# Kernel tuning notes

Measured on AMD Instinct MI355X. Metric: run time of the kernel, lower is better.

Reference implementation:

```python
import jax, jax.numpy as jnp
import numpy as np

R = 32  # voxel resolution


def setup_inputs() -> dict:
    key = jax.random.key(0)
    k1, k2 = jax.random.split(key)
    B, C, N = 8, 64, 100000
    features = jax.random.normal(k1, (B, C, N), dtype=jnp.float32)
    coords = jax.random.uniform(k2, (B, 3, N), dtype=jnp.float32)  # unit cube [0,1]
    return {"features": features, "coords": coords}


def reference(features, coords):
    # features: [B, C, N], coords: [B, 3, N] in [0, 1]
    B, C, N = features.shape
    norm_coords = jnp.clip(coords * R, 0, R - 1)
    vox_coords = jnp.round(norm_coords).astype(jnp.int32)  # [B, 3, N]

    # flat voxel index per point: x*R^2 + y*R + z, offset per batch
    idx = vox_coords[:, 0] * R * R + vox_coords[:, 1] * R + vox_coords[:, 2]  # [B, N]
    flat_idx = (idx + jnp.arange(B, dtype=jnp.int32)[:, None] * (R ** 3)).reshape(-1)  # [B*N]

    feat = jnp.transpose(features, (0, 2, 1)).reshape(B * N, C)  # [B*N, C]
    sums = jax.ops.segment_sum(feat, flat_idx, num_segments=B * R ** 3)  # [B*R^3, C]
    cnt = jax.ops.segment_sum(jnp.ones((B * N,), features.dtype), flat_idx,
                              num_segments=B * R ** 3)  # [B*R^3]
    avg = sums / jnp.maximum(cnt, 1.0)[:, None]  # average; empty voxels stay 0

    vox_feat = jnp.transpose(avg.reshape(B, R ** 3, C), (0, 2, 1)).reshape(B, C, R, R, R)
    return vox_feat, vox_coords.astype(jnp.int64)
```

## Files before the change

kernel.cpp:

```cpp
#include <hip/hip_runtime.h>

#define RR 32
#define R3 32768
#define BATCH 8
#define CH 64
#define NPTS 100000
#define NPOINTS (BATCH * NPTS)
#define NVOX (BATCH * R3)
#define SCAN_BLOCKS (NVOX / 256)

typedef unsigned int uint32;

__device__ __forceinline__ uint32 f2bf(float f) {
    uint32 u = __float_as_uint(f);
    return (u + 0x7fffu + ((u >> 16) & 1u)) >> 16;
}
__device__ __forceinline__ float bf2f(uint32 h) {
    return __uint_as_float(h << 16);
}

__global__ __launch_bounds__(256) void phase1_count(
    const float* __restrict__ coords,
    uint32* __restrict__ vox,
    uint32* __restrict__ cnt,
    float* __restrict__ out2)
{
    int gid = blockIdx.x * blockDim.x + threadIdx.x;
    if (gid >= NPOINTS) return;
    int b = gid / NPTS;
    int n = gid - b * NPTS;

    const float* cb = coords + (size_t)b * 3 * NPTS + n;
    float fx = fminf(fmaxf(cb[0]        * 32.0f, 0.0f), 31.0f);
    float fy = fminf(fmaxf(cb[NPTS]     * 32.0f, 0.0f), 31.0f);
    float fz = fminf(fmaxf(cb[2 * NPTS] * 32.0f, 0.0f), 31.0f);
    int x = (int)rintf(fx);
    int y = (int)rintf(fy);
    int z = (int)rintf(fz);
    uint32 g = (uint32)(b * R3 + x * (RR * RR) + y * RR + z);

    float* o2 = out2 + (size_t)b * 3 * NPTS + n;
    o2[0]        = (float)x;
    o2[NPTS]     = (float)y;
    o2[2 * NPTS] = (float)z;

    vox[gid] = g;
    atomicAdd(&cnt[g], 1u);
}

__global__ __launch_bounds__(256) void scan_block_sums(
    const uint32* __restrict__ cnt, uint32* __restrict__ bsum)
{
    __shared__ uint32 s[256];
    int t = threadIdx.x;
    s[t] = cnt[blockIdx.x * 256 + t];
    __syncthreads();
    for (int off = 128; off > 0; off >>= 1) {
        if (t < off) s[t] += s[t + off];
        __syncthreads();
    }
    if (t == 0) bsum[blockIdx.x] = s[0];
}

__global__ __launch_bounds__(256) void scan_bsum(uint32* __restrict__ bsum)
{
    __shared__ uint32 s[256];
    int t = threadIdx.x;
    uint32 v0 = bsum[4 * t], v1 = bsum[4 * t + 1], v2 = bsum[4 * t + 2], v3 = bsum[4 * t + 3];
    uint32 tot = v0 + v1 + v2 + v3;
    s[t] = tot;
    __syncthreads();
    for (int off = 1; off < 256; off <<= 1) {
        uint32 x = (t >= off) ? s[t - off] : 0u;
        __syncthreads();
        s[t] += x;
        __syncthreads();
    }
    uint32 excl = s[t] - tot;
    bsum[4 * t]     = excl;
    bsum[4 * t + 1] = excl + v0;
    bsum[4 * t + 2] = excl + v0 + v1;
    bsum[4 * t + 3] = excl + v0 + v1 + v2;
}

__global__ __launch_bounds__(256) void scan_final(
    const uint32* __restrict__ cnt, const uint32* __restrict__ bsum,
    uint32* __restrict__ starts, uint32* __restrict__ cursor)
{
    __shared__ uint32 s[256];
    int t = threadIdx.x;
    int gid = blockIdx.x * 256 + t;
    uint32 v = cnt[gid];
    s[t] = v;
    __syncthreads();
    for (int off = 1; off < 256; off <<= 1) {
        uint32 x = (t >= off) ? s[t - off] : 0u;
        __syncthreads();
        s[t] += x;
        __syncthreads();
    }
    uint32 st = bsum[blockIdx.x] + s[t] - v;
    starts[gid] = st;
    cursor[gid] = st;
}

__global__ __launch_bounds__(256) void phase3_scatter(
    const float* __restrict__ feat,
    const uint32* __restrict__ vox,
    uint32* __restrict__ cursor,
    uint4* __restrict__ sorted)
{
    int gid = blockIdx.x * blockDim.x + threadIdx.x;
    if (gid >= NPOINTS) return;
    int b = gid / NPTS;
    int n = gid - b * NPTS;

    uint32 g = vox[gid];
    uint32 pos = atomicAdd(&cursor[g], 1u);

    const float* frow = feat + (size_t)b * CH * NPTS + n;
    uint4* dst = sorted + (size_t)pos * 8;
#pragma unroll
    for (int j = 0; j < 8; ++j) {
        uint4 w;
        float f0 = frow[(size_t)(8 * j + 0) * NPTS];
        float f1 = frow[(size_t)(8 * j + 1) * NPTS];
        float f2 = frow[(size_t)(8 * j + 2) * NPTS];
        float f3 = frow[(size_t)(8 * j + 3) * NPTS];
        float f4 = frow[(size_t)(8 * j + 4) * NPTS];
        float f5 = frow[(size_t)(8 * j + 5) * NPTS];
        float f6 = frow[(size_t)(8 * j + 6) * NPTS];
        float f7 = frow[(size_t)(8 * j + 7) * NPTS];
        w.x = f2bf(f0) | (f2bf(f1) << 16);
        w.y = f2bf(f2) | (f2bf(f3) << 16);
        w.z = f2bf(f4) | (f2bf(f5) << 16);
        w.w = f2bf(f6) | (f2bf(f7) << 16);
        dst[j] = w;
    }
}

__global__ __launch_bounds__(256) void phase4_reduce(
    const uint32* __restrict__ sorted,
    const uint32* __restrict__ starts,
    float* __restrict__ out1)
{
    __shared__ float tile[64][65];

    int gbase = blockIdx.x * 64;
    int tid = threadIdx.x;
    int wave = tid >> 6, lane = tid & 63;

    if (lane < 32) {
        for (int k = 0; k < 16; ++k) {
            int g = gbase + wave * 16 + k;
            uint32 s = starts[g];
            uint32 e = (g == NVOX - 1) ? (uint32)NPOINTS : starts[g + 1];
            float a0 = 0.0f, a1 = 0.0f;
            for (uint32 p = s; p < e; ++p) {
                uint32 w = sorted[(size_t)p * 32 + lane];
                a0 += bf2f(w & 0xffffu);
                a1 += bf2f(w >> 16);
            }
            uint32 c = e - s;
            float rcp = 1.0f / (float)(c > 1u ? c : 1u);
            int vloc = wave * 16 + k;
            tile[vloc][2 * lane]     = a0 * rcp;
            tile[vloc][2 * lane + 1] = a1 * rcp;
        }
    }
    __syncthreads();

    int b = gbase / R3;
    int v0 = gbase - b * R3;
    int vv = tid & 63;
    int c0 = tid >> 6;
    float* obase = out1 + (size_t)b * CH * R3 + v0 + vv;
#pragma unroll
    for (int jj = 0; jj < 16; ++jj) {
        int c = jj * 4 + c0;
        obase[(size_t)c * R3] = tile[vv][c];
    }
}

__global__ __launch_bounds__(256) void accum_direct(
    const float* __restrict__ feat, const float* __restrict__ coords,
    float* __restrict__ out1, uint32* __restrict__ cnt, float* __restrict__ out2)
{
    int gid = blockIdx.x * blockDim.x + threadIdx.x;
    if (gid >= NPOINTS) return;
    int b = gid / NPTS;
    int n = gid - b * NPTS;
    const float* cb = coords + (size_t)b * 3 * NPTS + n;
    float fx = fminf(fmaxf(cb[0]        * 32.0f, 0.0f), 31.0f);
    float fy = fminf(fmaxf(cb[NPTS]     * 32.0f, 0.0f), 31.0f);
    float fz = fminf(fmaxf(cb[2 * NPTS] * 32.0f, 0.0f), 31.0f);
    int x = (int)rintf(fx), y = (int)rintf(fy), z = (int)rintf(fz);
    int v = x * (RR * RR) + y * RR + z;
    float* o2 = out2 + (size_t)b * 3 * NPTS + n;
    o2[0] = (float)x; o2[NPTS] = (float)y; o2[2 * NPTS] = (float)z;
    atomicAdd(&cnt[b * R3 + v], 1u);
    float* obase = out1 + (size_t)(b * CH) * R3 + v;
    const float* frow = feat + (size_t)(b * CH) * NPTS + n;
#pragma unroll 8
    for (int c = 0; c < CH; ++c)
        unsafeAtomicAdd(&obase[(size_t)c * R3], frow[(size_t)c * NPTS]);
}

__global__ __launch_bounds__(256) void finalize_direct(
    float* __restrict__ out1, const uint32* __restrict__ cnt)
{
    size_t gid = (size_t)blockIdx.x * blockDim.x + threadIdx.x;
    size_t total = (size_t)BATCH * CH * R3;
    if (gid >= total) return;
    int v = (int)(gid & (R3 - 1));
    int b = (int)(gid / ((size_t)CH * R3));
    uint32 ct = cnt[b * R3 + v];
    out1[gid] = out1[gid] / (float)(ct > 1u ? ct : 1u);
}

extern "C" void kernel_launch(void* const* d_in, const int* in_sizes, int n_in,
                              void* d_out, int out_size, void* d_ws, size_t ws_size,
                              hipStream_t stream)
{
    const float* feat   = (const float*)d_in[0];
    const float* coords = (const float*)d_in[1];

    float* out1 = (float*)d_out;
    float* out2 = out1 + (size_t)BATCH * CH * R3;

    const size_t vox_off    = 0;
    const size_t vox_bytes  = (size_t)NPOINTS * 4;
    const size_t cnt_off    = vox_off + ((vox_bytes + 255) & ~255ull);
    const size_t cnt_bytes  = (size_t)NVOX * 4;
    const size_t starts_off = cnt_off + ((cnt_bytes + 255) & ~255ull);
    const size_t cursor_off = starts_off + ((cnt_bytes + 255) & ~255ull);
    const size_t bsum_off   = cursor_off + ((cnt_bytes + 255) & ~255ull);
    const size_t bsum_bytes = (size_t)SCAN_BLOCKS * 4;
    const size_t sort_off   = (bsum_off + bsum_bytes + 255) & ~255ull;
    const size_t sort_bytes = (size_t)NPOINTS * 128;
    const size_t need       = sort_off + sort_bytes;

    const int npt_blocks = (NPOINTS + 255) / 256;

    if (ws_size >= need) {
        char* ws = (char*)d_ws;
        uint32* vox    = (uint32*)(ws + vox_off);
        uint32* cnt    = (uint32*)(ws + cnt_off);
        uint32* starts = (uint32*)(ws + starts_off);
        uint32* cursor = (uint32*)(ws + cursor_off);
        uint32* bsum   = (uint32*)(ws + bsum_off);
        uint32* sorted = (uint32*)(ws + sort_off);

        hipMemsetAsync(cnt, 0, cnt_bytes, stream);
        phase1_count<<<npt_blocks, 256, 0, stream>>>(coords, vox, cnt, out2);
        scan_block_sums<<<SCAN_BLOCKS, 256, 0, stream>>>(cnt, bsum);
        scan_bsum<<<1, 256, 0, stream>>>(bsum);
        scan_final<<<SCAN_BLOCKS, 256, 0, stream>>>(cnt, bsum, starts, cursor);
        phase3_scatter<<<npt_blocks, 256, 0, stream>>>(feat, vox, cursor, (uint4*)sorted);
        phase4_reduce<<<NVOX / 64, 256, 0, stream>>>(sorted, starts, out1);
    } else {
        uint32* cnt = (uint32*)d_ws;
        hipMemsetAsync(out1, 0, (size_t)BATCH * CH * R3 * sizeof(float), stream);
        hipMemsetAsync(d_ws, 0, (size_t)NVOX * 4, stream);
        accum_direct<<<npt_blocks, 256, 0, stream>>>(feat, coords, out1, cnt, out2);
        size_t total = (size_t)BATCH * CH * R3;
        finalize_direct<<<(unsigned)((total + 255) / 256), 256, 0, stream>>>(out1, cnt);
    }
}
```

Before: 498.8 us.

## Process point pairs with vector loads and use 16-byte reads in voxel reduction

The count and scatter kernels now handle two consecutive points per thread, using 8-byte vector loads and stores for coords, features and voxel ids, plus nontemporal hints on the feature reads and sorted-buffer writes. The reduce kernel has all 64 lanes active: each 8-lane group handles one voxel and reads 16 bytes per lane per point, instead of 32 lanes doing 4-byte reads. This is meant to cut memory transactions and idle lanes. It halves the thread count in the point kernels and adds more per-thread register pressure.

```diff
diff --git a/kernel.cpp b/kernel.cpp
--- a/kernel.cpp
+++ b/kernel.cpp
@@ -10,6 +10,9 @@
 #define SCAN_BLOCKS (NVOX / 256)
 
 typedef unsigned int uint32;
+typedef unsigned int uintx4 __attribute__((ext_vector_type(4)));
+typedef unsigned int uintx2 __attribute__((ext_vector_type(2)));
+typedef float floatx2 __attribute__((ext_vector_type(2)));
 
 __device__ __forceinline__ uint32 f2bf(float f) {
     uint32 u = __float_as_uint(f);
@@ -25,27 +28,35 @@
     uint32* __restrict__ cnt,
     float* __restrict__ out2)
 {
-    int gid = blockIdx.x * blockDim.x + threadIdx.x;
-    if (gid >= NPOINTS) return;
-    int b = gid / NPTS;
-    int n = gid - b * NPTS;
+    int pid = blockIdx.x * blockDim.x + threadIdx.x;
+    if (pid >= NPOINTS / 2) return;
+    int p0 = pid * 2;
+    int b = p0 / NPTS;
+    int n = p0 - b * NPTS;
 
     const float* cb = coords + (size_t)b * 3 * NPTS + n;
-    float fx = fminf(fmaxf(cb[0]        * 32.0f, 0.0f), 31.0f);
-    float fy = fminf(fmaxf(cb[NPTS]     * 32.0f, 0.0f), 31.0f);
-    float fz = fminf(fmaxf(cb[2 * NPTS] * 32.0f, 0.0f), 31.0f);
-    int x = (int)rintf(fx);
-    int y = (int)rintf(fy);
-    int z = (int)rintf(fz);
-    uint32 g = (uint32)(b * R3 + x * (RR * RR) + y * RR + z);
+    floatx2 cx = *(const floatx2*)(cb);
+    floatx2 cy = *(const floatx2*)(cb + NPTS);
+    floatx2 cz = *(const floatx2*)(cb + 2 * NPTS);
+
+    int x0 = (int)rintf(fminf(fmaxf(cx.x * 32.0f, 0.0f), 31.0f));
+    int y0 = (int)rintf(fminf(fmaxf(cy.x * 32.0f, 0.0f), 31.0f));
+    int z0 = (int)rintf(fminf(fmaxf(cz.x * 32.0f, 0.0f), 31.0f));
+    int x1 = (int)rintf(fminf(fmaxf(cx.y * 32.0f, 0.0f), 31.0f));
+    int y1 = (int)rintf(fminf(fmaxf(cy.y * 32.0f, 0.0f), 31.0f));
+    int z1 = (int)rintf(fminf(fmaxf(cz.y * 32.0f, 0.0f), 31.0f));
+
+    uint32 g0 = (uint32)(b * R3 + x0 * (RR * RR) + y0 * RR + z0);
+    uint32 g1 = (uint32)(b * R3 + x1 * (RR * RR) + y1 * RR + z1);
 
     float* o2 = out2 + (size_t)b * 3 * NPTS + n;
-    o2[0]        = (float)x;
-    o2[NPTS]     = (float)y;
-    o2[2 * NPTS] = (float)z;
-
-    vox[gid] = g;
-    atomicAdd(&cnt[g], 1u);
+    *(floatx2*)(o2)            = floatx2{(float)x0, (float)x1};
+    *(floatx2*)(o2 + NPTS)     = floatx2{(float)y0, (float)y1};
+    *(floatx2*)(o2 + 2 * NPTS) = floatx2{(float)z0, (float)z1};
+
+    *(uintx2*)(vox + p0) = uintx2{g0, g1};
+    atomicAdd(&cnt[g0], 1u);
+    atomicAdd(&cnt[g1], 1u);
 }
 
 __global__ __launch_bounds__(256) void scan_block_sums(
@@ -108,34 +119,40 @@
     const float* __restrict__ feat,
     const uint32* __restrict__ vox,
     uint32* __restrict__ cursor,
-    uint4* __restrict__ sorted)
-{
-    int gid = blockIdx.x * blockDim.x + threadIdx.x;
-    if (gid >= NPOINTS) return;
-    int b = gid / NPTS;
-    int n = gid - b * NPTS;
-
-    uint32 g = vox[gid];
-    uint32 pos = atomicAdd(&cursor[g], 1u);
+    uintx4* __restrict__ sorted)
+{
+    int pid = blockIdx.x * blockDim.x + threadIdx.x;
+    if (pid >= NPOINTS / 2) return;
+    int p0 = pid * 2;
+    int b = p0 / NPTS;
+    int n = p0 - b * NPTS;
+
+    uintx2 gg = *(const uintx2*)(vox + p0);
+    uint32 pos0 = atomicAdd(&cursor[gg.x], 1u);
+    uint32 pos1 = atomicAdd(&cursor[gg.y], 1u);
 
     const float* frow = feat + (size_t)b * CH * NPTS + n;
-    uint4* dst = sorted + (size_t)pos * 8;
+    uintx4* d0 = sorted + (size_t)pos0 * 8;
+    uintx4* d1 = sorted + (size_t)pos1 * 8;
+
 #pragma unroll
     for (int j = 0; j < 8; ++j) {
-        uint4 w;
-        float f0 = frow[(size_t)(8 * j + 0) * NPTS];
-        float f1 = frow[(size_t)(8 * j + 1) * NPTS];
-        float f2 = frow[(size_t)(8 * j + 2) * NPTS];
-        float f3 = frow[(size_t)(8 * j + 3) * NPTS];
-        float f4 = frow[(size_t)(8 * j + 4) * NPTS];
-        float f5 = frow[(size_t)(8 * j + 5) * NPTS];
-        float f6 = frow[(size_t)(8 * j + 6) * NPTS];
-        float f7 = frow[(size_t)(8 * j + 7) * NPTS];
-        w.x = f2bf(f0) | (f2bf(f1) << 16);
-        w.y = f2bf(f2) | (f2bf(f3) << 16);
-        w.z = f2bf(f4) | (f2bf(f5) << 16);
-        w.w = f2bf(f6) | (f2bf(f7) << 16);
-        dst[j] = w;
+        floatx2 f[8];
+#pragma unroll
+        for (int i = 0; i < 8; ++i)
+            f[i] = __builtin_nontemporal_load(
+                (const floatx2*)(frow + (size_t)(8 * j + i) * NPTS));
+        uintx4 w0, w1;
+        w0.x = f2bf(f[0].x) | (f2bf(f[1].x) << 16);
+        w0.y = f2bf(f[2].x) | (f2bf(f[3].x) << 16);
+        w0.z = f2bf(f[4].x) | (f2bf(f[5].x) << 16);
+        w0.w = f2bf(f[6].x) | (f2bf(f[7].x) << 16);
+        w1.x = f2bf(f[0].y) | (f2bf(f[1].y) << 16);
+        w1.y = f2bf(f[2].y) | (f2bf(f[3].y) << 16);
+        w1.z = f2bf(f[4].y) | (f2bf(f[5].y) << 16);
+        w1.w = f2bf(f[6].y) | (f2bf(f[7].y) << 16);
+        __builtin_nontemporal_store(w0, d0 + j);
+        __builtin_nontemporal_store(w1, d1 + j);
     }
 }
 
@@ -148,30 +165,37 @@
 
     int gbase = blockIdx.x * 64;
     int tid = threadIdx.x;
-    int wave = tid >> 6, lane = tid & 63;
-
-    if (lane < 32) {
-        for (int k = 0; k < 16; ++k) {
-            int g = gbase + wave * 16 + k;
-            uint32 s = starts[g];
-            uint32 e = (g == NVOX - 1) ? (uint32)NPOINTS : starts[g + 1];
-            float a0 = 0.0f, a1 = 0.0f;
-            for (uint32 p = s; p < e; ++p) {
-                uint32 w = sorted[(size_t)p * 32 + lane];
-                a0 += bf2f(w & 0xffffu);
-                a1 += bf2f(w >> 16);
-            }
-            uint32 c = e - s;
-            float rcp = 1.0f / (float)(c > 1u ? c : 1u);
-            int vloc = wave * 16 + k;
-            tile[vloc][2 * lane]     = a0 * rcp;
-            tile[vloc][2 * lane + 1] = a1 * rcp;
+    int w = tid >> 6, lane = tid & 63;
+    int gq = lane >> 3, l8 = lane & 7;
+
+#pragma unroll
+    for (int iter = 0; iter < 2; ++iter) {
+        int vloc = w * 16 + iter * 8 + gq;
+        int g = gbase + vloc;
+        uint32 s = starts[g];
+        uint32 e = (g == NVOX - 1) ? (uint32)NPOINTS : starts[g + 1];
+        float a0 = 0.f, a1 = 0.f, a2 = 0.f, a3 = 0.f;
+        float a4 = 0.f, a5 = 0.f, a6 = 0.f, a7 = 0.f;
+        for (uint32 p = s; p < e; ++p) {
+            uintx4 wv = __builtin_nontemporal_load(
+                (const uintx4*)(sorted + (size_t)p * 32) + l8);
+            a0 += bf2f(wv.x & 0xffffu); a1 += bf2f(wv.x >> 16);
+            a2 += bf2f(wv.y & 0xffffu); a3 += bf2f(wv.y >> 16);
+            a4 += bf2f(wv.z & 0xffffu); a5 += bf2f(wv.z >> 16);
+            a6 += bf2f(wv.w & 0xffffu); a7 += bf2f(wv.w >> 16);
         }
+        uint32 c = e - s;
+        float rcp = 1.0f / (float)(c > 1u ? c : 1u);
+        float* trow = &tile[vloc][l8 * 8];
+        trow[0] = a0 * rcp; trow[1] = a1 * rcp;
+        trow[2] = a2 * rcp; trow[3] = a3 * rcp;
+        trow[4] = a4 * rcp; trow[5] = a5 * rcp;
+        trow[6] = a6 * rcp; trow[7] = a7 * rcp;
     }
     __syncthreads();
 
     int b = gbase / R3;
-    int v0 = gbase - b * R3;
+    int v0 = gbase & (R3 - 1);
     int vv = tid & 63;
     int c0 = tid >> 6;
     float* obase = out1 + (size_t)b * CH * R3 + v0 + vv;
@@ -240,7 +264,7 @@
     const size_t sort_bytes = (size_t)NPOINTS * 128;
     const size_t need       = sort_off + sort_bytes;
 
-    const int npt_blocks = (NPOINTS + 255) / 256;
+    const int pair_blocks = (NPOINTS / 2 + 255) / 256;
 
     if (ws_size >= need) {
         char* ws = (char*)d_ws;
@@ -251,18 +275,18 @@
         uint32* bsum   = (uint32*)(ws + bsum_off);
         uint32* sorted = (uint32*)(ws + sort_off);
 
-        hipMemsetAsync(cnt, 0, cnt_bytes, stream);
-        phase1_count<<<npt_blocks, 256, 0, stream>>>(coords, vox, cnt, out2);
+        (void)hipMemsetAsync(cnt, 0, cnt_bytes, stream);
+        phase1_count<<<pair_blocks, 256, 0, stream>>>(coords, vox, cnt, out2);
         scan_block_sums<<<SCAN_BLOCKS, 256, 0, stream>>>(cnt, bsum);
         scan_bsum<<<1, 256, 0, stream>>>(bsum);
         scan_final<<<SCAN_BLOCKS, 256, 0, stream>>>(cnt, bsum, starts, cursor);
-        phase3_scatter<<<npt_blocks, 256, 0, stream>>>(feat, vox, cursor, (uint4*)sorted);
+        phase3_scatter<<<pair_blocks, 256, 0, stream>>>(feat, vox, cursor, (uintx4*)sorted);
         phase4_reduce<<<NVOX / 64, 256, 0, stream>>>(sorted, starts, out1);
     } else {
         uint32* cnt = (uint32*)d_ws;
-        hipMemsetAsync(out1, 0, (size_t)BATCH * CH * R3 * sizeof(float), stream);
-        hipMemsetAsync(d_ws, 0, (size_t)NVOX * 4, stream);
-        accum_direct<<<npt_blocks, 256, 0, stream>>>(feat, coords, out1, cnt, out2);
+        (void)hipMemsetAsync(out1, 0, (size_t)BATCH * CH * R3 * sizeof(float), stream);
+        (void)hipMemsetAsync(d_ws, 0, (size_t)NVOX * 4, stream);
+        accum_direct<<<(NPOINTS + 255) / 256, 256, 0, stream>>>(feat, coords, out1, cnt, out2);
         size_t total = (size_t)BATCH * CH * R3;
         finalize_direct<<<(unsigned)((total + 255) / 256), 256, 0, stream>>>(out1, cnt);
     }
```

Measured after the change: 605.3 us. +21.4%, slower.
